# Kernel optimization log

Hardware: AMD Instinct MI355X
Metric: run time of the kernel (lower is better)

Reference implementation:

```python
import jax, jax.numpy as jnp
import numpy as np

TEMP = 0.07


def setup_inputs() -> dict:
    key = jax.random.key(0)
    kq, kk = jax.random.split(key)
    B, D = 8192, 128
    q = jax.random.normal(kq, (B, D), dtype=jnp.float32)
    k = jax.random.normal(kk, (B, D), dtype=jnp.float32)
    return {"q": q, "k": k}


def reference(q, k):
    # features = cat([q, k], dim=0); F.normalize(dim=1)
    B = q.shape[0]
    N = 2 * B
    f = jnp.concatenate([q, k], axis=0)
    f = f / jnp.maximum(jnp.linalg.norm(f, axis=1, keepdims=True), 1e-12)
    sim = f @ f.T  # [N, N]

    i = jnp.arange(N)
    p = (i + B) % N                      # index of the positive pair of row i
    pos = sim[i, p][:, None]             # [N, 1]

    # negatives: all columns except the diagonal (i) and the positive (p),
    # in original column order (matches boolean-mask ordering in torch).
    a = jnp.minimum(i, p)[:, None]       # [N, 1]
    b = jnp.maximum(i, p)[:, None]
    j = jnp.arange(N - 2)[None, :]       # [1, N-2]
    c = j + (j >= a)                     # skip first excluded column
    c = c + (c >= b)                     # skip second excluded column
    neg = jnp.take_along_axis(sim, c, axis=1)  # [N, N-2]

    logits = jnp.concatenate([pos, neg], axis=1) / TEMP  # [N, N-1]
    labels = jnp.zeros((N,), dtype=jnp.int32)
    return logits, labels
```

## Files before the change

### kernel.cpp

```cpp
#include <hip/hip_runtime.h>
#include <hip/hip_bf16.h>
#include <stdint.h>

#define B_ROWS 8192
#define N_TOT  16384
#define D_DIM  128
#define SCALE_SQRT_INVT 3.7796447300922722f

typedef __bf16 bf16x8 __attribute__((ext_vector_type(8)));
typedef float  f32x4  __attribute__((ext_vector_type(4)));

__global__ void simclr_norm_kernel(const float* __restrict__ q,
                                   const float* __restrict__ k,
                                   unsigned int* __restrict__ fb) {
    const int lane = threadIdx.x & 63;
    const int row  = blockIdx.x * 4 + (threadIdx.x >> 6);
    const float* src = (row < B_ROWS) ? (q + (size_t)row * D_DIM)
                                      : (k + (size_t)(row - B_ROWS) * D_DIM);
    float2 v = ((const float2*)src)[lane];
    float s = v.x * v.x + v.y * v.y;
#pragma unroll
    for (int off = 32; off > 0; off >>= 1) s += __shfl_xor(s, off);
    float rn = SCALE_SQRT_INVT / fmaxf(sqrtf(s), 1e-12f);
    union { __bf16 h[2]; unsigned int u; } pk;
    pk.h[0] = (__bf16)(v.x * rn);
    pk.h[1] = (__bf16)(v.y * rn);
    fb[(size_t)row * 64 + lane] = pk.u;
}

__global__ __launch_bounds__(256, 2) void simclr_gemm_kernel(
        const unsigned short* __restrict__ fb, float* __restrict__ out) {
    __shared__ char lds[65536];

    const int bid = blockIdx.x;
    const int r0  = (bid >> 1) * 64;
    const int h   = bid & 1;
    const int tid  = threadIdx.x;
    const int lane = tid & 63;
    const int w    = tid >> 6;
    const int rl = lane & 15;
    const int kg = lane >> 4;

    const char* fbb = (const char*)fb;

    auto stage = [&](int buf, int t) {
        const int c0 = h * 8192 + t * 128;
#pragma unroll
        for (int rnd = 0; rnd < 8; ++rnd) {
            const int row   = rnd * 16 + w * 4 + (lane >> 4);
            const int chunk = (lane & 15) ^ (row & 7);
            const char* g = fbb + (size_t)(c0 + row) * 256 + chunk * 16;
            char* l = lds + buf * 32768 + (rnd * 16 + w * 4) * 256;
            __builtin_amdgcn_global_load_lds((const __attribute__((address_space(1))) void*)g,
                                             (__attribute__((address_space(3))) void*)l, 16, 0, 0);
        }
    };

    stage(0, 0);

    bf16x8 afr[4][4];
#pragma unroll
    for (int m = 0; m < 4; ++m)
#pragma unroll
        for (int ks = 0; ks < 4; ++ks)
            afr[m][ks] = *(const bf16x8*)(fbb + (size_t)(r0 + m * 16 + rl) * 256 + ks * 64 + kg * 16);

    for (int t = 0; t < 64; ++t) {
        const int cur = t & 1;

        if (t < 63) {
            stage(cur ^ 1, t + 1);
            asm volatile("s_waitcnt vmcnt(16)" ::: "memory");
        } else {
            asm volatile("s_waitcnt vmcnt(8)" ::: "memory");
        }
        __builtin_amdgcn_sched_barrier(0);
        __builtin_amdgcn_s_barrier();
        __builtin_amdgcn_sched_barrier(0);

        bf16x8 bfr[4][2];
#pragma unroll
        for (int ks = 0; ks < 4; ++ks) {
            const int kb = ks * 64 + kg * 16;
#pragma unroll
            for (int n = 0; n < 2; ++n) {
                const int rr = w * 32 + n * 16 + rl;
                bfr[ks][n] = *(const bf16x8*)(lds + cur * 32768 + rr * 256 + (kb ^ ((rr & 7) << 4)));
            }
        }
        asm volatile("s_waitcnt lgkmcnt(0)" ::: "memory");
        __builtin_amdgcn_sched_barrier(0);
        __builtin_amdgcn_s_barrier();
        __builtin_amdgcn_sched_barrier(0);

        f32x4 acc[4][2];
#pragma unroll
        for (int m = 0; m < 4; ++m)
#pragma unroll
            for (int n = 0; n < 2; ++n) acc[m][n] = (f32x4){0.f, 0.f, 0.f, 0.f};
#pragma unroll
        for (int ks = 0; ks < 4; ++ks)
#pragma unroll
            for (int m = 0; m < 4; ++m)
#pragma unroll
                for (int n = 0; n < 2; ++n)
                    acc[m][n] = __builtin_amdgcn_mfma_f32_16x16x32_bf16(bfr[ks][n], afr[m][ks], acc[m][n], 0, 0, 0);

        const int c0 = h * 8192 + t * 128;
        const int cw = c0 + w * 32 + (kg << 2);
#pragma unroll
        for (int m = 0; m < 4; ++m) {
            const int i = r0 + m * 16 + rl;
            const int p = i ^ B_ROWS;
            const int a = i & (B_ROWS - 1);
            const int b = a | B_ROWS;
            float* orow = out + (size_t)i * (N_TOT - 1);
#pragma unroll
            for (int n = 0; n < 2; ++n) {
                const int c = cw + n * 16;
                f32x4 v = acc[m][n];
                if (__builtin_expect((unsigned)(a - c) < 4u || (unsigned)(b - c) < 4u, 0)) {
#pragma unroll
                    for (int e = 0; e < 4; ++e) {
                        const int cc = c + e;
                        const float val = v[e];
                        if (cc == i) continue;
                        if (cc == p) { orow[0] = val; continue; }
                        orow[cc + 1 - (cc > a) - (cc > b)] = val;
                    }
                } else {
                    const int s = 1 - (c > a) - (c > b);
                    __builtin_memcpy(orow + c + s, &v, sizeof(v));
                }
            }
        }
    }
}

__global__ void simclr_zero_labels(float* __restrict__ out) {
    out[(size_t)N_TOT * (N_TOT - 1) + blockIdx.x * 256 + threadIdx.x] = 0.0f;
}

extern "C" void kernel_launch(void* const* d_in, const int* in_sizes, int n_in,
                              void* d_out, int out_size, void* d_ws, size_t ws_size,
                              hipStream_t stream) {
    const float* q = (const float*)d_in[0];
    const float* k = (const float*)d_in[1];
    float* out = (float*)d_out;
    unsigned int* fb = (unsigned int*)d_ws;

    simclr_norm_kernel<<<N_TOT / 4, 256, 0, stream>>>(q, k, fb);
    simclr_zero_labels<<<N_TOT / 256, 256, 0, stream>>>(out);
    simclr_gemm_kernel<<<512, 256, 0, stream>>>((const unsigned short*)d_ws, out);
}
```

Baseline: 360.5 us.

## Load B fragments directly to registers and stage output through LDS for coalesced stores

Drops the LDS double-buffered async staging of the B tile. B fragments are now loaded straight from global memory into registers, with a register prefetch of the next tile. The freed LDS is used to transpose each 64x128 accumulator tile so that each half-wave writes 512 contiguous bytes of one output row, instead of scattered 16-byte stores across 16 rows. The goal is better write coalescing on the store-bound output, at the cost of an extra LDS round trip and two barriers per iteration, plus uncoalesced direct global loads for B.

```diff
diff --git a/kernel.cpp b/kernel.cpp
--- a/kernel.cpp
+++ b/kernel.cpp
@@ -30,33 +30,19 @@
 
 __global__ __launch_bounds__(256, 2) void simclr_gemm_kernel(
         const unsigned short* __restrict__ fb, float* __restrict__ out) {
-    __shared__ char lds[65536];
+    __shared__ char lds[32768];
 
     const int bid = blockIdx.x;
     const int r0  = (bid >> 1) * 64;
     const int h   = bid & 1;
-    const int tid  = threadIdx.x;
-    const int lane = tid & 63;
-    const int w    = tid >> 6;
+    const int lane = threadIdx.x & 63;
+    const int w    = threadIdx.x >> 6;
     const int rl = lane & 15;
     const int kg = lane >> 4;
 
     const char* fbb = (const char*)fb;
-
-    auto stage = [&](int buf, int t) {
-        const int c0 = h * 8192 + t * 128;
-#pragma unroll
-        for (int rnd = 0; rnd < 8; ++rnd) {
-            const int row   = rnd * 16 + w * 4 + (lane >> 4);
-            const int chunk = (lane & 15) ^ (row & 7);
-            const char* g = fbb + (size_t)(c0 + row) * 256 + chunk * 16;
-            char* l = lds + buf * 32768 + (rnd * 16 + w * 4) * 256;
-            __builtin_amdgcn_global_load_lds((const __attribute__((address_space(1))) void*)g,
-                                             (__attribute__((address_space(3))) void*)l, 16, 0, 0);
-        }
-    };
-
-    stage(0, 0);
+    const int cbase = h * 8192;
+    const int base_s = (h == 0) ? 1 : 0;
 
     bf16x8 afr[4][4];
 #pragma unroll
@@ -65,32 +51,23 @@
         for (int ks = 0; ks < 4; ++ks)
             afr[m][ks] = *(const bf16x8*)(fbb + (size_t)(r0 + m * 16 + rl) * 256 + ks * 64 + kg * 16);
 
+    bf16x8 bcur[4][2], bnxt[4][2];
+#pragma unroll
+    for (int ks = 0; ks < 4; ++ks)
+#pragma unroll
+        for (int n = 0; n < 2; ++n)
+            bcur[ks][n] = *(const bf16x8*)(fbb + (size_t)(cbase + w * 32 + n * 16 + rl) * 256 + ks * 64 + kg * 16);
+
     for (int t = 0; t < 64; ++t) {
-        const int cur = t & 1;
+        const int c0 = cbase + t * 128;
 
         if (t < 63) {
-            stage(cur ^ 1, t + 1);
-            asm volatile("s_waitcnt vmcnt(16)" ::: "memory");
-        } else {
-            asm volatile("s_waitcnt vmcnt(8)" ::: "memory");
+#pragma unroll
+            for (int ks = 0; ks < 4; ++ks)
+#pragma unroll
+                for (int n = 0; n < 2; ++n)
+                    bnxt[ks][n] = *(const bf16x8*)(fbb + (size_t)(c0 + 128 + w * 32 + n * 16 + rl) * 256 + ks * 64 + kg * 16);
         }
-        __builtin_amdgcn_sched_barrier(0);
-        __builtin_amdgcn_s_barrier();
-        __builtin_amdgcn_sched_barrier(0);
-
-        bf16x8 bfr[4][2];
-#pragma unroll
-        for (int ks = 0; ks < 4; ++ks) {
-            const int kb = ks * 64 + kg * 16;
-#pragma unroll
-            for (int n = 0; n < 2; ++n) {
-                const int rr = w * 32 + n * 16 + rl;
-                bfr[ks][n] = *(const bf16x8*)(lds + cur * 32768 + rr * 256 + (kb ^ ((rr & 7) << 4)));
-            }
-        }
-        asm volatile("s_waitcnt lgkmcnt(0)" ::: "memory");
-        __builtin_amdgcn_sched_barrier(0);
-        __builtin_amdgcn_s_barrier();
         __builtin_amdgcn_sched_barrier(0);
 
         f32x4 acc[4][2];
@@ -104,35 +81,55 @@
             for (int m = 0; m < 4; ++m)
 #pragma unroll
                 for (int n = 0; n < 2; ++n)
-                    acc[m][n] = __builtin_amdgcn_mfma_f32_16x16x32_bf16(bfr[ks][n], afr[m][ks], acc[m][n], 0, 0, 0);
+                    acc[m][n] = __builtin_amdgcn_mfma_f32_16x16x32_bf16(bcur[ks][n], afr[m][ks], acc[m][n], 0, 0, 0);
 
-        const int c0 = h * 8192 + t * 128;
-        const int cw = c0 + w * 32 + (kg << 2);
 #pragma unroll
         for (int m = 0; m < 4; ++m) {
-            const int i = r0 + m * 16 + rl;
-            const int p = i ^ B_ROWS;
-            const int a = i & (B_ROWS - 1);
-            const int b = a | B_ROWS;
-            float* orow = out + (size_t)i * (N_TOT - 1);
+            const int row = m * 16 + rl;
 #pragma unroll
             for (int n = 0; n < 2; ++n) {
-                const int c = cw + n * 16;
-                f32x4 v = acc[m][n];
-                if (__builtin_expect((unsigned)(a - c) < 4u || (unsigned)(b - c) < 4u, 0)) {
+                const int colb = w * 128 + n * 64 + kg * 16;
+                *(f32x4*)(lds + row * 512 + (colb ^ ((row & 7) << 4))) = acc[m][n];
+            }
+        }
+        asm volatile("s_waitcnt lgkmcnt(0)" ::: "memory");
+        __builtin_amdgcn_sched_barrier(0);
+        __builtin_amdgcn_s_barrier();
+        __builtin_amdgcn_sched_barrier(0);
+
 #pragma unroll
-                    for (int e = 0; e < 4; ++e) {
-                        const int cc = c + e;
-                        const float val = v[e];
-                        if (cc == i) continue;
-                        if (cc == p) { orow[0] = val; continue; }
-                        orow[cc + 1 - (cc > a) - (cc > b)] = val;
-                    }
-                } else {
-                    const int s = 1 - (c > a) - (c > b);
-                    __builtin_memcpy(orow + c + s, &v, sizeof(v));
+        for (int j = 0; j < 8; ++j) {
+            const int row = w * 16 + j * 2 + (lane >> 5);
+            const int i   = r0 + row;
+            const int ch  = lane & 31;
+            f32x4 v = *(const f32x4*)(lds + row * 512 + ((ch * 16) ^ ((row & 7) << 4)));
+            const int sc = cbase + (i & (B_ROWS - 1));
+            float* orow = out + (size_t)i * (N_TOT - 1);
+            const unsigned rel = (unsigned)(sc - c0);
+            if (__builtin_expect(rel < 128u, 0)) {
+                const bool isdiag = ((i >> 13) == h);
+#pragma unroll
+                for (int e = 0; e < 4; ++e) {
+                    const int c = c0 + ch * 4 + e;
+                    const float val = v[e];
+                    if (c == sc) { if (!isdiag) orow[0] = val; }
+                    else orow[c + base_s - (c > sc)] = val;
                 }
+            } else {
+                const int s = base_s - (c0 > sc ? 1 : 0);
+                __builtin_memcpy(orow + c0 + s + ch * 4, &v, sizeof(v));
             }
+        }
+        __builtin_amdgcn_sched_barrier(0);
+        __builtin_amdgcn_s_barrier();
+        __builtin_amdgcn_sched_barrier(0);
+
+        if (t < 63) {
+#pragma unroll
+            for (int ks = 0; ks < 4; ++ks)
+#pragma unroll
+                for (int n = 0; n < 2; ++n)
+                    bcur[ks][n] = bnxt[ks][n];
         }
     }
 }
```

Measured after the change: 362.3 us. No clear change (+0.5%).
